# Kernel optimization log

Measured on AMD Instinct MI355X. Metric: run time of the kernel, lower is better.

## Reference

```python
import jax, jax.numpy as jnp
import numpy as np

C, H, W = 8, 8, 8
A = 6            # action_dim
LATENT = 64
HID = 64
GRU_IN = HID + A + LATENT  # 134


def _conv(x, w):
    return jax.lax.conv_general_dilated(
        x, w, (1, 1), 'VALID', dimension_numbers=('NCHW', 'OIHW', 'NCHW'))


def setup_inputs() -> dict:
    key = jax.random.key(0)
    ks = jax.random.split(key, 20)
    B, N, T = 64, 10, 128
    s_h = jax.random.normal(ks[0], (B, N, T, C, H, W), jnp.float32)
    a_h = jax.random.randint(ks[1], (B, N, T), 0, A).astype(jnp.int64)
    b_z = jax.random.normal(ks[2], (B, LATENT), jnp.float32)
    s = 0.05
    p = {
        'conv1_w': jax.random.normal(ks[3], (32, C, 3, 3)) * s,
        'conv1_b': jnp.zeros((32,)),
        'conv2_w': jax.random.normal(ks[4], (32, 32, 3, 3)) * s,
        'conv2_b': jnp.zeros((32,)),
        'fc_w': jax.random.normal(ks[5], (HID, 32 * 4 * 4)) * s,
        'fc_b': jnp.zeros((HID,)),
        'emb': jax.random.normal(ks[6], (A, A)) * s,
        'gru_wih': jax.random.normal(ks[7], (3 * HID, GRU_IN)) * s,
        'gru_whh': jax.random.normal(ks[8], (3 * HID, HID)) * s,
        'gru_bih': jnp.zeros((3 * HID,)),
        'gru_bhh': jnp.zeros((3 * HID,)),
        'mlp1_w': jax.random.normal(ks[9], (HID, HID)) * s,
        'mlp1_b': jnp.zeros((HID,)),
        'mlp2_w': jax.random.normal(ks[10], (A, HID)) * s,
        'mlp2_b': jnp.zeros((A,)),
    }
    return {'s_h': s_h, 'a_h': a_h, 'b_z': b_z, **p}


def reference(s_h, a_h, b_z, conv1_w, conv1_b, conv2_w, conv2_b, fc_w, fc_b,
              emb, gru_wih, gru_whh, gru_bih, gru_bhh,
              mlp1_w, mlp1_b, mlp2_w, mlp2_b):
    B, N = s_h.shape[0], s_h.shape[1]
    T = a_h.shape[2]
    BN = B * N

    # action mask, [B, N, T, 1]
    action_masks = (a_h != A - 1)[..., None].astype(jnp.float32)

    # --- state encoder on first frame only ---
    s0 = s_h[:, :, 0].reshape(BN, C, H, W)
    x = jax.nn.relu(_conv(s0, conv1_w) + conv1_b[:, None, None])
    x = jax.nn.relu(_conv(x, conv2_w) + conv2_b[:, None, None])
    x = x.reshape(BN, -1)                       # [BN, 512]
    state_emb = jax.nn.relu(x @ fc_w.T + fc_b)  # [BN, HID]

    bz = jnp.broadcast_to(b_z[:, None, :], (B, N, LATENT)).reshape(BN, LATENT)

    h0 = jnp.zeros((BN, HID), s_h.dtype)
    act0 = jnp.full((BN,), A - 1, jnp.int32)

    def step(carry, _):
        h, act = carry
        a_emb = emb[act]                                          # [BN, A]
        inp = jnp.concatenate([state_emb, a_emb, bz], axis=-1)    # [BN, GRU_IN]
        gx = inp @ gru_wih.T + gru_bih
        gh = h @ gru_whh.T + gru_bhh
        xr, xz, xn = jnp.split(gx, 3, axis=-1)
        hr, hz, hn = jnp.split(gh, 3, axis=-1)
        r = jax.nn.sigmoid(xr + hr)
        z = jax.nn.sigmoid(xz + hz)
        n = jnp.tanh(xn + r * hn)
        h_new = (1.0 - z) * n + z * h
        hid = jnp.tanh(h_new @ mlp1_w.T + mlp1_b)
        logits = hid @ mlp2_w.T + mlp2_b                          # [BN, A]
        next_act = jax.lax.stop_gradient(jnp.argmax(logits, axis=-1)).astype(jnp.int32)
        return (h_new, next_act), logits

    (_, _), logits_seq = jax.lax.scan(step, (h0, act0), None, length=T - 1)
    # logits_seq: [T-1, BN, A] -> [B, N, T-1, A]
    logits_all = jnp.transpose(logits_seq, (1, 0, 2)).reshape(B, N, T - 1, A)
    return logits_all, action_masks
```

## Files before the change

### kernel.cpp

```cpp
#include <hip/hip_runtime.h>

#define A_DIM 6
#define HID_D 64
#define LATENT_D 64
#define GRU_IN_D 134
#define T_STEPS 128
#define N_ENV 10
#define BN_TOT 640

typedef float f2 __attribute__((ext_vector_type(2)));

__device__ __forceinline__ float fast_sigmoid(float x) {
    return __builtin_amdgcn_rcpf(1.0f + __builtin_amdgcn_exp2f(-1.4426950408889634f * x));
}
__device__ __forceinline__ float fast_tanh(float x) {
    return 1.0f - 2.0f * __builtin_amdgcn_rcpf(1.0f + __builtin_amdgcn_exp2f(2.8853900817779268f * x));
}

template<int CTRL>
__device__ __forceinline__ float dppadd(float v) {
    int t = __builtin_amdgcn_update_dpp(0, __builtin_bit_cast(int, v), CTRL, 0xf, 0xf, true);
    return v + __builtin_bit_cast(float, t);
}
__device__ __forceinline__ float wave_reduce_add(float v) {
    v = dppadd<0x111>(v);
    v = dppadd<0x112>(v);
    v = dppadd<0x114>(v);
    v = dppadd<0x118>(v);
    v = dppadd<0x142>(v);
    v = dppadd<0x143>(v);
    return __builtin_bit_cast(float, __builtin_amdgcn_readlane(__builtin_bit_cast(int, v), 63));
}

__global__ __launch_bounds__(128, 1)
void policy_kernel(const float* __restrict__ s_h,
                   const int*   __restrict__ a_h,
                   const float* __restrict__ b_z,
                   const float* __restrict__ conv1_w, const float* __restrict__ conv1_b,
                   const float* __restrict__ conv2_w, const float* __restrict__ conv2_b,
                   const float* __restrict__ fc_w,    const float* __restrict__ fc_b,
                   const float* __restrict__ emb,
                   const float* __restrict__ gru_wih, const float* __restrict__ gru_whh,
                   const float* __restrict__ gru_bih, const float* __restrict__ gru_bhh,
                   const float* __restrict__ mlp1_w,  const float* __restrict__ mlp1_b,
                   const float* __restrict__ mlp2_w,  const float* __restrict__ mlp2_b,
                   float* __restrict__ logits_out, float* __restrict__ mask_out)
{
    __shared__ __align__(16) float s0[512];
    __shared__ __align__(16) float a1[1152];
    __shared__ __align__(16) float a2[512];
    __shared__ __align__(16) float pfc[128];
    __shared__ __align__(16) float semb[64];
    __shared__ __align__(16) float gxc[192];
    __shared__ __align__(16) float atab[6*192];
    __shared__ __align__(16) float hspec[6*64];
    __shared__ __align__(16) float llog[(T_STEPS-1)*A_DIM];

    const int bn  = blockIdx.x;
    const int tid = threadIdx.x;
    const int j   = tid & 63;
    const int w   = tid >> 6;

    mask_out[bn * T_STEPS + tid] = (a_h[bn * T_STEPS + tid] != (A_DIM - 1)) ? 1.0f : 0.0f;

    {
        const float* src = s_h + (size_t)bn * T_STEPS * 512;
        #pragma unroll
        for (int i = 0; i < 4; ++i) s0[tid + i * 128] = src[tid + i * 128];
    }
    __syncthreads();

    for (int i = tid; i < 1152; i += 128) {
        const int oc = i / 36, r = i % 36, oh = r / 6, ow = r % 6;
        float sum = conv1_b[oc];
        const float* wp = conv1_w + oc * 72;
        #pragma unroll
        for (int ic = 0; ic < 8; ++ic)
            #pragma unroll
            for (int kh = 0; kh < 3; ++kh)
                #pragma unroll
                for (int kw = 0; kw < 3; ++kw)
                    sum = fmaf(s0[ic * 64 + (oh + kh) * 8 + (ow + kw)],
                               wp[ic * 9 + kh * 3 + kw], sum);
        a1[i] = fmaxf(sum, 0.0f);
    }
    __syncthreads();

    for (int i = tid; i < 512; i += 128) {
        const int oc = i / 16, r = i % 16, oh = r / 4, ow = r % 4;
        float sum = conv2_b[oc];
        const float* wp = conv2_w + oc * 288;
        for (int ic = 0; ic < 32; ++ic)
            #pragma unroll
            for (int kh = 0; kh < 3; ++kh)
                #pragma unroll
                for (int kw = 0; kw < 3; ++kw)
                    sum = fmaf(a1[ic * 36 + (oh + kh) * 6 + (ow + kw)],
                               wp[ic * 9 + kh * 3 + kw], sum);
        a2[i] = fmaxf(sum, 0.0f);
    }
    __syncthreads();

    {
        const float* wp = fc_w + j * 512 + w * 256;
        const float* ap = a2 + w * 256;
        float s0a = 0.f, s1a = 0.f, s2a = 0.f, s3a = 0.f;
        for (int k = 0; k < 256; k += 4) {
            s0a = fmaf(ap[k + 0], wp[k + 0], s0a);
            s1a = fmaf(ap[k + 1], wp[k + 1], s1a);
            s2a = fmaf(ap[k + 2], wp[k + 2], s2a);
            s3a = fmaf(ap[k + 3], wp[k + 3], s3a);
        }
        pfc[tid] = (s0a + s1a) + (s2a + s3a);
    }
    __syncthreads();
    if (tid < 64) semb[tid] = fmaxf(pfc[tid] + pfc[tid + 64] + fc_b[tid], 0.0f);
    __syncthreads();

    {
        const float* bz = b_z + (size_t)(bn / N_ENV) * LATENT_D;
        for (int g = tid; g < 192; g += 128) {
            float sum = gru_bih[g] + ((g < 128) ? gru_bhh[g] : 0.0f);
            const float* wp = gru_wih + g * GRU_IN_D;
            for (int k = 0; k < 64; ++k) sum = fmaf(semb[k], wp[k], sum);
            for (int k = 0; k < 64; ++k) sum = fmaf(bz[k], wp[70 + k], sum);
            gxc[g] = sum;
        }
    }
    for (int i = tid; i < 6 * 192; i += 128) {
        const int a = i / 192, g = i % 192;
        float sum = 0.0f;
        #pragma unroll
        for (int q = 0; q < 6; ++q)
            sum = fmaf(emb[a * 6 + q], gru_wih[g * GRU_IN_D + 64 + q], sum);
        atab[i] = sum;
    }
    __syncthreads();

    if (w == 1) return;

    f2 wr[32], wz[32], wn[32], w1[32];
    {
        const float* pr = gru_whh + (size_t)j * 64;
        const float* pz = gru_whh + (size_t)(64 + j) * 64;
        const float* pn = gru_whh + (size_t)(128 + j) * 64;
        const float* p1 = mlp1_w + (size_t)j * 64;
        #pragma unroll
        for (int i = 0; i < 16; ++i) {
            float4 v;
            v = ((const float4*)pr)[i]; wr[2*i] = (f2){v.x, v.y}; wr[2*i+1] = (f2){v.z, v.w};
            v = ((const float4*)pz)[i]; wz[2*i] = (f2){v.x, v.y}; wz[2*i+1] = (f2){v.z, v.w};
            v = ((const float4*)pn)[i]; wn[2*i] = (f2){v.x, v.y}; wn[2*i+1] = (f2){v.z, v.w};
            v = ((const float4*)p1)[i]; w1[2*i] = (f2){v.x, v.y}; w1[2*i+1] = (f2){v.z, v.w};
        }
    }
    const float bhn = gru_bhh[128 + j];
    const float b1j = mlp1_b[j];
    float arx[6], azx[6], anx[6], m2c[6], b2[6];
    {
        const float gxr = gxc[j], gxz = gxc[64 + j], gxn = gxc[128 + j];
        #pragma unroll
        for (int a = 0; a < 6; ++a) {
            arx[a] = gxr + atab[a * 192 + j];
            azx[a] = gxz + atab[a * 192 + 64 + j];
            anx[a] = gxn + atab[a * 192 + 128 + j];
            m2c[a] = mlp2_w[a * 64 + j];
            b2[a] = mlp2_b[a];
        }
    }

    float ha[6];
    #pragma unroll
    for (int a = 0; a < 6; ++a) {
        const float r = fast_sigmoid(arx[a]);
        const float z = fast_sigmoid(azx[a]);
        const float n = fast_tanh(fmaf(r, bhn, anx[a]));
        ha[a] = fmaf(z, 0.0f - n, n);
    }
    __builtin_amdgcn_wave_barrier();
    #pragma unroll
    for (int a = 0; a < 6; ++a) hspec[a * 64 + j] = ha[a];
    __builtin_amdgcn_wave_barrier();

    int act = A_DIM - 1;

    for (int t = 0; t < T_STEPS - 1; ++t) {
        const float4* hb = (const float4*)(hspec + (act << 6));
        float hprev = ha[0];
        #pragma unroll
        for (int a = 1; a < 6; ++a) hprev = (act == a) ? ha[a] : hprev;

        float4 h00 = hb[0],  h01 = hb[1],  h02 = hb[2],  h03 = hb[3];
        float4 h04 = hb[4],  h05 = hb[5],  h06 = hb[6],  h07 = hb[7];
        float4 h08 = hb[8],  h09 = hb[9],  h10 = hb[10], h11 = hb[11];
        float4 h12 = hb[12], h13 = hb[13], h14 = hb[14], h15 = hb[15];
        __builtin_amdgcn_sched_barrier(0);

        f2 p1a = {0.f, 0.f}, p1b = {0.f, 0.f};
        f2 pr = {0.f, 0.f}, pz = {0.f, 0.f}, pn = {0.f, 0.f};
        #define SWEEP(i, hv) { \
            const f2 haa = (f2){hv.x, hv.y}; \
            const f2 hcc = (f2){hv.z, hv.w}; \
            p1a += haa * w1[2*(i)]; p1b += hcc * w1[2*(i)+1]; \
            pr += haa * wr[2*(i)]; pr += hcc * wr[2*(i)+1]; \
            pz += haa * wz[2*(i)]; pz += hcc * wz[2*(i)+1]; \
            pn += haa * wn[2*(i)]; pn += hcc * wn[2*(i)+1]; }
        SWEEP(0,  h00) SWEEP(1,  h01) SWEEP(2,  h02) SWEEP(3,  h03)
        SWEEP(4,  h04) SWEEP(5,  h05) SWEEP(6,  h06) SWEEP(7,  h07)
        SWEEP(8,  h08) SWEEP(9,  h09) SWEEP(10, h10) SWEEP(11, h11)
        SWEEP(12, h12) SWEEP(13, h13) SWEEP(14, h14) SWEEP(15, h15)
        #undef SWEEP
        const f2 p1 = p1a + p1b;
        const float hid = fast_tanh(p1.x + p1.y + b1j);
        const float hr = pr.x + pr.y;
        const float hz = pz.x + pz.y;
        const float hn = pn.x + pn.y + bhn;

        const float l0 = wave_reduce_add(hid * m2c[0]) + b2[0];
        const float l1 = wave_reduce_add(hid * m2c[1]) + b2[1];
        const float l2 = wave_reduce_add(hid * m2c[2]) + b2[2];
        const float l3 = wave_reduce_add(hid * m2c[3]) + b2[3];
        const float l4 = wave_reduce_add(hid * m2c[4]) + b2[4];
        const float l5 = wave_reduce_add(hid * m2c[5]) + b2[5];

        #pragma unroll
        for (int a = 0; a < 6; ++a) {
            const float r = fast_sigmoid(arx[a] + hr);
            const float z = fast_sigmoid(azx[a] + hz);
            const float n = fast_tanh(fmaf(r, hn, anx[a]));
            ha[a] = fmaf(z, hprev - n, n);
        }
        __builtin_amdgcn_wave_barrier();
        #pragma unroll
        for (int a = 0; a < 6; ++a) hspec[a * 64 + j] = ha[a];
        __builtin_amdgcn_wave_barrier();

        float best = l0; int bi = 0;
        if (l1 > best) { best = l1; bi = 1; }
        if (l2 > best) { best = l2; bi = 2; }
        if (l3 > best) { best = l3; bi = 3; }
        if (l4 > best) { best = l4; bi = 4; }
        if (l5 > best) { best = l5; bi = 5; }
        act = bi;

        if (j < A_DIM) {
            const float outv = (j == 0) ? l0 : (j == 1) ? l1 : (j == 2) ? l2
                             : (j == 3) ? l3 : (j == 4) ? l4 : l5;
            llog[t * A_DIM + j] = outv;
        }
    }

    {
        float* lout = logits_out + (size_t)bn * (T_STEPS - 1) * A_DIM;
        for (int i = j; i < (T_STEPS - 1) * A_DIM; i += 64) lout[i] = llog[i];
    }
}

extern "C" void kernel_launch(void* const* d_in, const int* in_sizes, int n_in,
                              void* d_out, int out_size, void* d_ws, size_t ws_size,
                              hipStream_t stream) {
    const float* s_h     = (const float*)d_in[0];
    const int*   a_h     = (const int*)  d_in[1];
    const float* b_z     = (const float*)d_in[2];
    const float* conv1_w = (const float*)d_in[3];
    const float* conv1_b = (const float*)d_in[4];
    const float* conv2_w = (const float*)d_in[5];
    const float* conv2_b = (const float*)d_in[6];
    const float* fc_w    = (const float*)d_in[7];
    const float* fc_b    = (const float*)d_in[8];
    const float* emb     = (const float*)d_in[9];
    const float* gru_wih = (const float*)d_in[10];
    const float* gru_whh = (const float*)d_in[11];
    const float* gru_bih = (const float*)d_in[12];
    const float* gru_bhh = (const float*)d_in[13];
    const float* mlp1_w  = (const float*)d_in[14];
    const float* mlp1_b  = (const float*)d_in[15];
    const float* mlp2_w  = (const float*)d_in[16];
    const float* mlp2_b  = (const float*)d_in[17];

    float* out = (float*)d_out;
    float* logits_out = out;
    float* mask_out   = out + (size_t)BN_TOT * (T_STEPS - 1) * A_DIM;

    policy_kernel<<<BN_TOT, 128, 0, stream>>>(
        s_h, a_h, b_z, conv1_w, conv1_b, conv2_w, conv2_b, fc_w, fc_b, emb,
        gru_wih, gru_whh, gru_bih, gru_bhh, mlp1_w, mlp1_b, mlp2_w, mlp2_b,
        logits_out, mask_out);
}
```

Before: 453.5 us.

## Replace speculative per-action GRU update with argmax-selected single update

Drops the speculative computation of the new hidden state for all six possible actions, along with the per-action LDS buffer. The step now does a tree argmax over the logits, selects the matching precomputed input-gate terms, and computes a single GRU update that is written to a 64-entry LDS vector. It also splits the matvec accumulators into more independent chains to shorten dependency latency. The trade-off is that the argmax and the select now sit on the serial critical path before the gate math, where the old version could overlap them. The pairwise tree comparison keeps first-index tie semantics.

Result: faster. 422.3 us (-6.9%).

```diff
diff --git a/kernel.cpp b/kernel.cpp
--- a/kernel.cpp
+++ b/kernel.cpp
@@ -53,7 +53,7 @@
     __shared__ __align__(16) float semb[64];
     __shared__ __align__(16) float gxc[192];
     __shared__ __align__(16) float atab[6*192];
-    __shared__ __align__(16) float hspec[6*64];
+    __shared__ __align__(16) float h_lds[64];
     __shared__ __align__(16) float llog[(T_STEPS-1)*A_DIM];
 
     const int bn  = blockIdx.x;
@@ -169,52 +169,57 @@
         }
     }
 
-    float ha[6];
-    #pragma unroll
-    for (int a = 0; a < 6; ++a) {
-        const float r = fast_sigmoid(arx[a]);
-        const float z = fast_sigmoid(azx[a]);
-        const float n = fast_tanh(fmaf(r, bhn, anx[a]));
-        ha[a] = fmaf(z, 0.0f - n, n);
+    float hprev;
+    {
+        const float r = fast_sigmoid(arx[5]);
+        const float z = fast_sigmoid(azx[5]);
+        const float n = fast_tanh(fmaf(r, bhn, anx[5]));
+        hprev = fmaf(z, 0.0f - n, n);
     }
     __builtin_amdgcn_wave_barrier();
-    #pragma unroll
-    for (int a = 0; a < 6; ++a) hspec[a * 64 + j] = ha[a];
+    h_lds[j] = hprev;
     __builtin_amdgcn_wave_barrier();
 
-    int act = A_DIM - 1;
-
     for (int t = 0; t < T_STEPS - 1; ++t) {
-        const float4* hb = (const float4*)(hspec + (act << 6));
-        float hprev = ha[0];
-        #pragma unroll
-        for (int a = 1; a < 6; ++a) hprev = (act == a) ? ha[a] : hprev;
-
+        const float4* hb = (const float4*)h_lds;
         float4 h00 = hb[0],  h01 = hb[1],  h02 = hb[2],  h03 = hb[3];
         float4 h04 = hb[4],  h05 = hb[5],  h06 = hb[6],  h07 = hb[7];
         float4 h08 = hb[8],  h09 = hb[9],  h10 = hb[10], h11 = hb[11];
         float4 h12 = hb[12], h13 = hb[13], h14 = hb[14], h15 = hb[15];
         __builtin_amdgcn_sched_barrier(0);
 
-        f2 p1a = {0.f, 0.f}, p1b = {0.f, 0.f};
-        f2 pr = {0.f, 0.f}, pz = {0.f, 0.f}, pn = {0.f, 0.f};
-        #define SWEEP(i, hv) { \
+        f2 p1a = {0.f,0.f}, p1b = {0.f,0.f}, p1c = {0.f,0.f}, p1d = {0.f,0.f};
+        f2 pra = {0.f,0.f}, prb = {0.f,0.f};
+        f2 pza = {0.f,0.f}, pzb = {0.f,0.f};
+        f2 pna = {0.f,0.f}, pnb = {0.f,0.f};
+        #define SWEEPA(i, hv) { \
             const f2 haa = (f2){hv.x, hv.y}; \
             const f2 hcc = (f2){hv.z, hv.w}; \
             p1a += haa * w1[2*(i)]; p1b += hcc * w1[2*(i)+1]; \
-            pr += haa * wr[2*(i)]; pr += hcc * wr[2*(i)+1]; \
-            pz += haa * wz[2*(i)]; pz += hcc * wz[2*(i)+1]; \
-            pn += haa * wn[2*(i)]; pn += hcc * wn[2*(i)+1]; }
-        SWEEP(0,  h00) SWEEP(1,  h01) SWEEP(2,  h02) SWEEP(3,  h03)
-        SWEEP(4,  h04) SWEEP(5,  h05) SWEEP(6,  h06) SWEEP(7,  h07)
-        SWEEP(8,  h08) SWEEP(9,  h09) SWEEP(10, h10) SWEEP(11, h11)
-        SWEEP(12, h12) SWEEP(13, h13) SWEEP(14, h14) SWEEP(15, h15)
-        #undef SWEEP
-        const f2 p1 = p1a + p1b;
+            pra += haa * wr[2*(i)]; prb += hcc * wr[2*(i)+1]; \
+            pza += haa * wz[2*(i)]; pzb += hcc * wz[2*(i)+1]; \
+            pna += haa * wn[2*(i)]; pnb += hcc * wn[2*(i)+1]; }
+        #define SWEEPB(i, hv) { \
+            const f2 haa = (f2){hv.x, hv.y}; \
+            const f2 hcc = (f2){hv.z, hv.w}; \
+            p1c += haa * w1[2*(i)]; p1d += hcc * w1[2*(i)+1]; \
+            pra += haa * wr[2*(i)]; prb += hcc * wr[2*(i)+1]; \
+            pza += haa * wz[2*(i)]; pzb += hcc * wz[2*(i)+1]; \
+            pna += haa * wn[2*(i)]; pnb += hcc * wn[2*(i)+1]; }
+        SWEEPA(0,  h00) SWEEPA(1,  h01) SWEEPA(2,  h02) SWEEPA(3,  h03)
+        SWEEPA(4,  h04) SWEEPA(5,  h05) SWEEPA(6,  h06) SWEEPA(7,  h07)
+        SWEEPB(8,  h08) SWEEPB(9,  h09) SWEEPB(10, h10) SWEEPB(11, h11)
+        SWEEPB(12, h12) SWEEPB(13, h13) SWEEPB(14, h14) SWEEPB(15, h15)
+        #undef SWEEPA
+        #undef SWEEPB
+        const f2 p1 = (p1a + p1b) + (p1c + p1d);
         const float hid = fast_tanh(p1.x + p1.y + b1j);
-        const float hr = pr.x + pr.y;
-        const float hz = pz.x + pz.y;
-        const float hn = pn.x + pn.y + bhn;
+        const f2 prf = pra + prb;
+        const f2 pzf = pza + pzb;
+        const f2 pnf = pna + pnb;
+        const float hr = prf.x + prf.y;
+        const float hz = pzf.x + pzf.y;
+        const float hn = pnf.x + pnf.y + bhn;
 
         const float l0 = wave_reduce_add(hid * m2c[0]) + b2[0];
         const float l1 = wave_reduce_add(hid * m2c[1]) + b2[1];
@@ -223,31 +228,46 @@
         const float l4 = wave_reduce_add(hid * m2c[4]) + b2[4];
         const float l5 = wave_reduce_add(hid * m2c[5]) + b2[5];
 
-        #pragma unroll
-        for (int a = 0; a < 6; ++a) {
-            const float r = fast_sigmoid(arx[a] + hr);
-            const float z = fast_sigmoid(azx[a] + hz);
-            const float n = fast_tanh(fmaf(r, hn, anx[a]));
-            ha[a] = fmaf(z, hprev - n, n);
-        }
-        __builtin_amdgcn_wave_barrier();
-        #pragma unroll
-        for (int a = 0; a < 6; ++a) hspec[a * 64 + j] = ha[a];
-        __builtin_amdgcn_wave_barrier();
-
-        float best = l0; int bi = 0;
-        if (l1 > best) { best = l1; bi = 1; }
-        if (l2 > best) { best = l2; bi = 2; }
-        if (l3 > best) { best = l3; bi = 3; }
-        if (l4 > best) { best = l4; bi = 4; }
-        if (l5 > best) { best = l5; bi = 5; }
-        act = bi;
-
         if (j < A_DIM) {
             const float outv = (j == 0) ? l0 : (j == 1) ? l1 : (j == 2) ? l2
                              : (j == 3) ? l3 : (j == 4) ? l4 : l5;
             llog[t * A_DIM + j] = outv;
         }
+
+        const bool c01 = l1 > l0;
+        const float m01 = c01 ? l1 : l0;
+        float sr = c01 ? arx[1] : arx[0];
+        float sz = c01 ? azx[1] : azx[0];
+        float sn = c01 ? anx[1] : anx[0];
+        const bool c23 = l3 > l2;
+        const float m23 = c23 ? l3 : l2;
+        const float sr23 = c23 ? arx[3] : arx[2];
+        const float sz23 = c23 ? azx[3] : azx[2];
+        const float sn23 = c23 ? anx[3] : anx[2];
+        const bool c45 = l5 > l4;
+        const float m45 = c45 ? l5 : l4;
+        const float sr45 = c45 ? arx[5] : arx[4];
+        const float sz45 = c45 ? azx[5] : azx[4];
+        const float sn45 = c45 ? anx[5] : anx[4];
+        const bool cA = m23 > m01;
+        const float mA = cA ? m23 : m01;
+        sr = cA ? sr23 : sr;
+        sz = cA ? sz23 : sz;
+        sn = cA ? sn23 : sn;
+        const bool cB = m45 > mA;
+        sr = cB ? sr45 : sr;
+        sz = cB ? sz45 : sz;
+        sn = cB ? sn45 : sn;
+
+        const float r = fast_sigmoid(sr + hr);
+        const float z = fast_sigmoid(sz + hz);
+        const float n = fast_tanh(fmaf(r, hn, sn));
+        const float hnew = fmaf(z, hprev - n, n);
+
+        __builtin_amdgcn_wave_barrier();
+        h_lds[j] = hnew;
+        hprev = hnew;
+        __builtin_amdgcn_wave_barrier();
     }
 
     {
```
